# Optimization experiments

Measured on AMD Instinct MI355X. Metric: run time of the kernel, lower is better.

## Reference

```python
import jax, jax.numpy as jnp
import numpy as np

N_ITER = 15
ITER_LR = 0.1


def setup_inputs() -> dict:
    key = jax.random.key(0)
    ks = jax.random.split(key, 4)
    dims = [784, 512, 256, 10]
    x = jax.random.normal(ks[0], (32768, dims[0]), dtype=jnp.float32)
    # weights[i]: (dims[i+1], dims[i]) scaled by sqrt(2/dims[i+1]); biases[i]: (dims[i],) zeros
    W0 = jax.random.normal(ks[1], (dims[1], dims[0]), dtype=jnp.float32) * np.sqrt(2.0 / dims[1]).astype(np.float32)
    W1 = jax.random.normal(ks[2], (dims[2], dims[1]), dtype=jnp.float32) * np.sqrt(2.0 / dims[2]).astype(np.float32)
    W2 = jax.random.normal(ks[3], (dims[3], dims[2]), dtype=jnp.float32) * np.sqrt(2.0 / dims[3]).astype(np.float32)
    b0 = jnp.zeros((dims[0],), dtype=jnp.float32)
    b1 = jnp.zeros((dims[1],), dtype=jnp.float32)
    b2 = jnp.zeros((dims[2],), dtype=jnp.float32)
    return {"x": x, "W0": W0, "W1": W1, "W2": W2, "b0": b0, "b1": b1, "b2": b2}


def reference(x, W0, W1, W2, b0, b1, b2):
    # feedforward pass: mus[i+1] = relu(mus[i] @ W[i].T)
    m1 = jax.nn.relu(x @ W0.T)    # [B, 512]
    m2 = jax.nn.relu(m1 @ W1.T)   # [B, 256]
    m3 = jax.nn.relu(m2 @ W2.T)   # [B, 10]

    # iterative predictive-coding updates: for l in {1, 2}:
    #   pred = relu(mus[l+1] @ W[l] + b[l]); mus[l] = relu(mus[l] - iter_lr * (mus[l] - pred))
    def body(_, carry):
        m1, m2, m3 = carry
        pred1 = jax.nn.relu(m2 @ W1 + b1)                 # uses m2 before its update (loop order)
        m1 = jax.nn.relu(m1 - ITER_LR * (m1 - pred1))
        pred2 = jax.nn.relu(m3 @ W2 + b2)
        m2 = jax.nn.relu(m2 - ITER_LR * (m2 - pred2))
        return (m1, m2, m3)

    m1, m2, m3 = jax.lax.fori_loop(0, N_ITER, body, (m1, m2, m3))
    # mus[-1] is never updated by the loop; returned as-is (faithful to the torch code)
    return m3
```

## Files before the change

kernel.cpp:

```cpp
#include <hip/hip_runtime.h>

typedef __bf16 bhalf;
typedef bhalf bhalf8 __attribute__((ext_vector_type(8)));
typedef float f32x4 __attribute__((ext_vector_type(4)));
typedef unsigned short u16;
typedef u16 u16x8 __attribute__((ext_vector_type(8)));

__device__ __forceinline__ u16 f2bf(float f) {
  union { float f; unsigned u; } v; v.f = f;
  unsigned r = v.u + 0x7FFFu + ((v.u >> 16) & 1u);
  return (u16)(r >> 16);
}

__device__ __forceinline__ int swz(int L) { return L ^ (((L >> 7) & 7) << 4); }

#define GLL16(gp, lp) __builtin_amdgcn_global_load_lds( \
    (const __attribute__((address_space(1))) unsigned int*)(gp), \
    (__attribute__((address_space(3))) unsigned int*)(lp), 16, 0, 0)

#define KP0 800
#define W0E (512 * KP0)
#define W1E (256 * 512)
#define W2E (16 * 256)

__global__ __launch_bounds__(256) void cvt_weights(
    const float* __restrict__ W0, const float* __restrict__ W1,
    const float* __restrict__ W2,
    u16* __restrict__ W0b, u16* __restrict__ W1b, u16* __restrict__ W2b)
{
  int i = blockIdx.x * 256 + threadIdx.x;
  if (i < W0E) {
    int r = i / KP0, k = i - r * KP0;
    W0b[i] = (k < 784) ? f2bf(W0[r * 784 + k]) : (u16)0;
    return;
  }
  i -= W0E;
  if (i < W1E) { W1b[i] = f2bf(W1[i]); return; }
  i -= W1E;
  if (i < W2E) {
    int r = i >> 8, c = i & 255;
    W2b[i] = (r < 10) ? f2bf(W2[r * 256 + c]) : (u16)0;
  }
}

__global__ __launch_bounds__(512) void gemm1_8p(
    const float* __restrict__ x, const u16* __restrict__ Wb, u16* __restrict__ Cp)
{
  __shared__ u16 lds[32768];
  const int t = threadIdx.x, w = t >> 6, lane = t & 63;
  const int bid = blockIdx.x;
  const int rt = (bid & 7) * 16 + (bid >> 4);
  const int ct = (bid >> 3) & 1;
  const size_t rbase = (size_t)rt * 256, cbase = (size_t)ct * 256;
  const int wr = w >> 2, wc = w & 3, fr = lane & 15, fg = lane >> 4;

  int aO[4], bO[4];
#pragma unroll
  for (int m = 0; m < 4; ++m) aO[m] = swz((wr * 128 + m * 16 + fr) * 64 + fg * 16);
#pragma unroll
  for (int n = 0; n < 4; ++n) bO[n] = swz((wc * 64 + n * 16 + fr) * 64 + fg * 16);

  const u16* bSrc[2];
#pragma unroll
  for (int i = 0; i < 2; ++i) {
    int P = (w * 2 + i) * 1024 + lane * 16;
    int U = swz(P);
    bSrc[i] = Wb + (size_t)(cbase + (U >> 6)) * KP0 + ((U & 63) >> 1);
  }

  const float* xRow[2]; int aKe[2];
#pragma unroll
  for (int c2 = 0; c2 < 2; ++c2) {
    int P = c2 * 8192 + t * 16;
    int U = swz(P);
    xRow[c2] = x + (size_t)(rbase + (U >> 6)) * 784;
    aKe[c2] = (U & 63) >> 1;
  }

  f32x4 acc[8][4];
#pragma unroll
  for (int m = 0; m < 8; ++m)
#pragma unroll
    for (int n = 0; n < 4; ++n) acc[m][n] = (f32x4){0.f, 0.f, 0.f, 0.f};

  f32x4 xr[2][2];
  bhalf8 bf[4], afA[4], afB[4];

  auto loadX = [&](int ttn) {
#pragma unroll
    for (int c2 = 0; c2 < 2; ++c2) {
      int gk = ttn * 32 + aKe[c2];
      const float* p = xRow[c2] + ((gk < 784) ? gk : 0);
      xr[c2][0] = *(const f32x4*)p; xr[c2][1] = *(const f32x4*)(p + 4);
    }
  };
  auto cvtW = [&](int aBaseOther) {
#pragma unroll
    for (int c2 = 0; c2 < 2; ++c2) {
      u16x8 v;
#pragma unroll
      for (int j = 0; j < 4; ++j) { v[j] = f2bf(xr[c2][0][j]); v[4 + j] = f2bf(xr[c2][1][j]); }
      *(u16x8*)((char*)lds + aBaseOther + c2 * 8192 + t * 16) = v;
    }
  };
  auto stageB = [&](int ttn, int bBaseT) {
#pragma unroll
    for (int i = 0; i < 2; ++i)
      GLL16(bSrc[i] + ttn * 32, (char*)lds + bBaseT + (w * 2 + i) * 1024);
  };
  auto rdB  = [&](int bB) {
#pragma unroll
    for (int n = 0; n < 4; ++n) bf[n] = *(const bhalf8*)((const char*)lds + bB + bO[n]);
  };
  auto rdA0 = [&](int aB) {
#pragma unroll
    for (int m = 0; m < 4; ++m) afA[m] = *(const bhalf8*)((const char*)lds + aB + aO[m]);
  };
  auto rdA1 = [&](int aB) {
#pragma unroll
    for (int m = 0; m < 4; ++m) afB[m] = *(const bhalf8*)((const char*)lds + aB + aO[m] + 4096);
  };
  auto mfmaLo = [&]() {
    __builtin_amdgcn_s_setprio(1);
#pragma unroll
    for (int m = 0; m < 4; ++m)
#pragma unroll
      for (int n = 0; n < 4; ++n)
        acc[m][n] = __builtin_amdgcn_mfma_f32_16x16x32_bf16(afA[m], bf[n], acc[m][n], 0, 0, 0);
    __builtin_amdgcn_s_setprio(0);
  };
  auto mfmaHi = [&]() {
    __builtin_amdgcn_s_setprio(1);
#pragma unroll
    for (int m = 0; m < 4; ++m)
#pragma unroll
      for (int n = 0; n < 4; ++n)
        acc[4 + m][n] = __builtin_amdgcn_mfma_f32_16x16x32_bf16(afB[m], bf[n], acc[4 + m][n], 0, 0, 0);
    __builtin_amdgcn_s_setprio(0);
  };

  loadX(0);
  stageB(0, 32768);
  cvtW(0);
  loadX(1);
  stageB(1, 49152);
  asm volatile("s_waitcnt vmcnt(6) lgkmcnt(0)" ::: "memory");
  __builtin_amdgcn_s_barrier();

  for (int tt = 0; tt < 23; ++tt) {
    const int c = tt & 1;
    const int aB = c << 14;
    const int bB = 32768 + (c << 14);
    rdB(bB); rdA0(aB); rdA1(aB);
    mfmaLo();
    asm volatile("s_waitcnt lgkmcnt(0)" ::: "memory");
    __builtin_amdgcn_s_barrier();
    cvtW(aB ^ 16384);
    loadX(tt + 2);
    stageB(tt + 2, bB);
    mfmaHi();
    asm volatile("s_waitcnt vmcnt(6) lgkmcnt(0)" ::: "memory");
    __builtin_amdgcn_s_barrier();
  }
  {
    rdB(49152); rdA0(16384); rdA1(16384);
    mfmaLo();
    asm volatile("s_waitcnt lgkmcnt(0)" ::: "memory");
    __builtin_amdgcn_s_barrier();
    cvtW(0);
    mfmaHi();
    asm volatile("s_waitcnt vmcnt(0) lgkmcnt(0)" ::: "memory");
    __builtin_amdgcn_s_barrier();

    rdB(32768); rdA0(0); rdA1(0);
    mfmaLo();
    rdA1(0);
    mfmaHi();
  }

#pragma unroll
  for (int m = 0; m < 8; ++m)
#pragma unroll
    for (int n = 0; n < 4; ++n)
#pragma unroll
      for (int q = 0; q < 4; ++q) {
        size_t row = rbase + wr * 128 + m * 16 + fg * 4 + q;
        size_t col = cbase + wc * 64 + n * 16 + fr;
        float vv = acc[m][n][q];
        vv = vv > 0.f ? vv : 0.f;
        Cp[row * 512 + col] = f2bf(vv);
      }
}

__global__ __launch_bounds__(512, 4) void gemm23(
    const u16* __restrict__ m1, const u16* __restrict__ W1b,
    const u16* __restrict__ W2b, float* __restrict__ out)
{
  __shared__ u16 pool[20480];
  __shared__ u16 W2s[16][264];
  const int t = threadIdx.x, w = t >> 6, lane = t & 63;
  const size_t rbase = (size_t)blockIdx.x * 64;
  const int wr = w >> 2, wc = w & 3, fr = lane & 15, fg = lane >> 4;

  {
    int r = t >> 5, kc = (t & 31) * 8;
    *(int4*)&W2s[r][kc] = *(const int4*)(W2b + r * 256 + kc);
  }

  int aOff[2], bOff[4];
#pragma unroll
  for (int i = 0; i < 2; ++i) aOff[i] = swz((wr * 32 + i * 16 + fr) * 64 + fg * 16);
#pragma unroll
  for (int j = 0; j < 4; ++j) bOff[j] = swz((wc * 64 + j * 16 + fr) * 64 + fg * 16);

  const u16* aSrc = nullptr; int aDst = 0;
  if (w < 4) {
    int Dl = (w * 64 + lane) * 16;
    int Ul = swz(Dl);
    aSrc = m1 + (rbase + (Ul >> 6)) * 512 + ((Ul & 63) >> 1);
    aDst = (w * 64) * 16;
  }
  const u16* bSrc[2]; int bDst[2];
#pragma unroll
  for (int i = 0; i < 2; ++i) {
    int Dl = (w * 128 + i * 64 + lane) * 16;
    int Ul = swz(Dl);
    bSrc[i] = W1b + (Ul >> 6) * 512 + ((Ul & 63) >> 1);
    bDst[i] = 8192 + (w * 128 + i * 64) * 16;
  }

  f32x4 acc[2][4];
#pragma unroll
  for (int i = 0; i < 2; ++i)
#pragma unroll
    for (int j = 0; j < 4; ++j) acc[i][j] = (f32x4){0.f, 0.f, 0.f, 0.f};

  if (w < 4) GLL16(aSrc, (char*)pool + aDst);
#pragma unroll
  for (int i = 0; i < 2; ++i) GLL16(bSrc[i], (char*)pool + bDst[i]);

  for (int tt = 0; tt < 16; ++tt) {
    const int cur = tt & 1;
    const char* Asc = (const char*)pool + cur * 4096;
    const char* Bsc = (const char*)pool + 8192 + cur * 16384;
    asm volatile("s_waitcnt vmcnt(0)" ::: "memory");
    __syncthreads();

    if (tt < 15) {
      const int k0 = (tt + 1) * 32;
      if (w < 4) GLL16(aSrc + k0, (char*)pool + (cur ^ 1) * 4096 + aDst);
#pragma unroll
      for (int i = 0; i < 2; ++i)
        GLL16(bSrc[i] + k0, (char*)pool + (cur ^ 1) * 16384 + bDst[i]);
    }

    bhalf8 af[2], bfv[4];
#pragma unroll
    for (int i = 0; i < 2; ++i) af[i] = *(const bhalf8*)(Asc + aOff[i]);
#pragma unroll
    for (int j = 0; j < 4; ++j) bfv[j] = *(const bhalf8*)(Bsc + bOff[j]);
#pragma unroll
    for (int i = 0; i < 2; ++i)
#pragma unroll
      for (int j = 0; j < 4; ++j)
        acc[i][j] = __builtin_amdgcn_mfma_f32_16x16x32_bf16(af[i], bfv[j], acc[i][j], 0, 0, 0);
  }

  __syncthreads();
#pragma unroll
  for (int i = 0; i < 2; ++i)
#pragma unroll
    for (int j = 0; j < 4; ++j)
#pragma unroll
      for (int q = 0; q < 4; ++q) {
        int row = wr * 32 + i * 16 + fg * 4 + q;
        int col = wc * 64 + j * 16 + fr;
        float vv = acc[i][j][q];
        vv = vv > 0.f ? vv : 0.f;
        pool[row * 264 + col] = f2bf(vv);
      }
  __syncthreads();

  if (w < 4) {
    f32x4 acc3 = (f32x4){0.f, 0.f, 0.f, 0.f};
    const int arow = w * 16 + fr;
#pragma unroll
    for (int ks = 0; ks < 8; ++ks) {
      bhalf8 a = *(const bhalf8*)&pool[arow * 264 + ks * 32 + fg * 8];
      bhalf8 b = *(const bhalf8*)&W2s[fr][ks * 32 + fg * 8];
      acc3 = __builtin_amdgcn_mfma_f32_16x16x32_bf16(a, b, acc3, 0, 0, 0);
    }
    if (fr < 10) {
#pragma unroll
      for (int q = 0; q < 4; ++q) {
        size_t row = rbase + w * 16 + fg * 4 + q;
        float vv = acc3[q];
        out[row * 10 + fr] = vv > 0.f ? vv : 0.f;
      }
    }
  }
}

extern "C" void kernel_launch(void* const* d_in, const int* in_sizes, int n_in,
                              void* d_out, int out_size, void* d_ws, size_t ws_size,
                              hipStream_t stream) {
  const float* x  = (const float*)d_in[0];
  const float* W0 = (const float*)d_in[1];
  const float* W1 = (const float*)d_in[2];
  const float* W2 = (const float*)d_in[3];
  float* out = (float*)d_out;

  char* ws = (char*)d_ws;
  u16* m1  = (u16*)(ws);
  u16* W0b = (u16*)(ws + 33554432);
  u16* W1b = (u16*)(ws + 34373632);
  u16* W2b = (u16*)(ws + 34635776);

  cvt_weights<<<dim3((W0E + W1E + W2E + 255) / 256), dim3(256), 0, stream>>>(
      W0, W1, W2, W0b, W1b, W2b);

  gemm1_8p<<<dim3(256), dim3(512), 0, stream>>>(x, W0b, m1);

  gemm23<<<dim3(512), dim3(512), 0, stream>>>(m1, W1b, W2b, out);
}
```

Baseline: 62.26 us.

## Retile first GEMM to full-width 128x512 tiles so each block reads x once

The first-layer GEMM changes from 256x256 output tiles (two column blocks per row tile) to 128-row tiles that span all 512 output columns. Each block now loads and converts its slice of the fp32 input exactly once, removing the duplicated x traffic and bf16 conversion that came from splitting columns across blocks. Each warp computes 4x8 MFMA fragments, and the B buffers grow, so LDS moves to 80KB of dynamic shared memory, set each launch through hipFuncSetAttribute. The cost is a larger per-block weight stream and heavier LDS use, which can limit occupancy to one block per CU.

```diff
diff --git a/kernel.cpp b/kernel.cpp
--- a/kernel.cpp
+++ b/kernel.cpp
@@ -43,82 +43,68 @@
   }
 }
 
-__global__ __launch_bounds__(512) void gemm1_8p(
+__global__ __launch_bounds__(512) void gemm1_fn(
     const float* __restrict__ x, const u16* __restrict__ Wb, u16* __restrict__ Cp)
 {
-  __shared__ u16 lds[32768];
+  extern __shared__ u16 lds[];
   const int t = threadIdx.x, w = t >> 6, lane = t & 63;
-  const int bid = blockIdx.x;
-  const int rt = (bid & 7) * 16 + (bid >> 4);
-  const int ct = (bid >> 3) & 1;
-  const size_t rbase = (size_t)rt * 256, cbase = (size_t)ct * 256;
+  const size_t rbase = (size_t)blockIdx.x * 128;
   const int wr = w >> 2, wc = w & 3, fr = lane & 15, fg = lane >> 4;
 
-  int aO[4], bO[4];
-#pragma unroll
-  for (int m = 0; m < 4; ++m) aO[m] = swz((wr * 128 + m * 16 + fr) * 64 + fg * 16);
-#pragma unroll
-  for (int n = 0; n < 4; ++n) bO[n] = swz((wc * 64 + n * 16 + fr) * 64 + fg * 16);
-
-  const u16* bSrc[2];
-#pragma unroll
-  for (int i = 0; i < 2; ++i) {
-    int P = (w * 2 + i) * 1024 + lane * 16;
+  int aO[4], bO[8];
+#pragma unroll
+  for (int m = 0; m < 4; ++m) aO[m] = swz((wr * 64 + m * 16 + fr) * 64 + fg * 16);
+#pragma unroll
+  for (int n = 0; n < 8; ++n) bO[n] = swz((wc * 128 + n * 16 + fr) * 64 + fg * 16);
+
+  const u16* bSrc[4];
+#pragma unroll
+  for (int i = 0; i < 4; ++i) {
+    int P = (w * 4 + i) * 1024 + lane * 16;
     int U = swz(P);
-    bSrc[i] = Wb + (size_t)(cbase + (U >> 6)) * KP0 + ((U & 63) >> 1);
-  }
-
-  const float* xRow[2]; int aKe[2];
-#pragma unroll
-  for (int c2 = 0; c2 < 2; ++c2) {
-    int P = c2 * 8192 + t * 16;
+    bSrc[i] = Wb + (size_t)(U >> 6) * KP0 + ((U & 63) >> 1);
+  }
+
+  const float* xRow; int aKe;
+  {
+    int P = t * 16;
     int U = swz(P);
-    xRow[c2] = x + (size_t)(rbase + (U >> 6)) * 784;
-    aKe[c2] = (U & 63) >> 1;
-  }
-
-  f32x4 acc[8][4];
-#pragma unroll
-  for (int m = 0; m < 8; ++m)
-#pragma unroll
-    for (int n = 0; n < 4; ++n) acc[m][n] = (f32x4){0.f, 0.f, 0.f, 0.f};
-
-  f32x4 xr[2][2];
-  bhalf8 bf[4], afA[4], afB[4];
-
-  auto loadX = [&](int ttn) {
-#pragma unroll
-    for (int c2 = 0; c2 < 2; ++c2) {
-      int gk = ttn * 32 + aKe[c2];
-      const float* p = xRow[c2] + ((gk < 784) ? gk : 0);
-      xr[c2][0] = *(const f32x4*)p; xr[c2][1] = *(const f32x4*)(p + 4);
-    }
-  };
-  auto cvtW = [&](int aBaseOther) {
-#pragma unroll
-    for (int c2 = 0; c2 < 2; ++c2) {
-      u16x8 v;
-#pragma unroll
-      for (int j = 0; j < 4; ++j) { v[j] = f2bf(xr[c2][0][j]); v[4 + j] = f2bf(xr[c2][1][j]); }
-      *(u16x8*)((char*)lds + aBaseOther + c2 * 8192 + t * 16) = v;
-    }
-  };
-  auto stageB = [&](int ttn, int bBaseT) {
-#pragma unroll
-    for (int i = 0; i < 2; ++i)
-      GLL16(bSrc[i] + ttn * 32, (char*)lds + bBaseT + (w * 2 + i) * 1024);
-  };
-  auto rdB  = [&](int bB) {
-#pragma unroll
-    for (int n = 0; n < 4; ++n) bf[n] = *(const bhalf8*)((const char*)lds + bB + bO[n]);
-  };
-  auto rdA0 = [&](int aB) {
+    xRow = x + (rbase + (U >> 6)) * (size_t)784;
+    aKe = (U & 63) >> 1;
+  }
+
+  f32x4 acc[4][8];
+#pragma unroll
+  for (int m = 0; m < 4; ++m)
+#pragma unroll
+    for (int n = 0; n < 8; ++n) acc[m][n] = (f32x4){0.f, 0.f, 0.f, 0.f};
+
+  f32x4 xr0, xr1;
+  bhalf8 bf[8], afA[4];
+
+  auto loadX = [&](int s) {
+    int gk = s * 32 + aKe;
+    const float* p = xRow + ((gk < 784) ? gk : 0);
+    xr0 = *(const f32x4*)p; xr1 = *(const f32x4*)(p + 4);
+  };
+  auto cvtW = [&](int aBase) {
+    u16x8 v;
+#pragma unroll
+    for (int j = 0; j < 4; ++j) { v[j] = f2bf(xr0[j]); v[4 + j] = f2bf(xr1[j]); }
+    *(u16x8*)((char*)lds + aBase + t * 16) = v;
+  };
+  auto stageB = [&](int s, int bBase) {
+#pragma unroll
+    for (int i = 0; i < 4; ++i)
+      GLL16(bSrc[i] + s * 32, (char*)lds + bBase + (w * 4 + i) * 1024);
+  };
+  auto rdA = [&](int aB) {
 #pragma unroll
     for (int m = 0; m < 4; ++m) afA[m] = *(const bhalf8*)((const char*)lds + aB + aO[m]);
   };
-  auto rdA1 = [&](int aB) {
-#pragma unroll
-    for (int m = 0; m < 4; ++m) afB[m] = *(const bhalf8*)((const char*)lds + aB + aO[m] + 4096);
+  auto rdB = [&](int bB) {
+#pragma unroll
+    for (int n = 0; n < 8; ++n) bf[n] = *(const bhalf8*)((const char*)lds + bB + bO[n]);
   };
   auto mfmaLo = [&]() {
     __builtin_amdgcn_s_setprio(1);
@@ -134,28 +120,28 @@
 #pragma unroll
     for (int m = 0; m < 4; ++m)
 #pragma unroll
-      for (int n = 0; n < 4; ++n)
-        acc[4 + m][n] = __builtin_amdgcn_mfma_f32_16x16x32_bf16(afB[m], bf[n], acc[4 + m][n], 0, 0, 0);
+      for (int n = 4; n < 8; ++n)
+        acc[m][n] = __builtin_amdgcn_mfma_f32_16x16x32_bf16(afA[m], bf[n], acc[m][n], 0, 0, 0);
     __builtin_amdgcn_s_setprio(0);
   };
 
   loadX(0);
-  stageB(0, 32768);
+  stageB(0, 16384);
   cvtW(0);
   loadX(1);
-  stageB(1, 49152);
+  stageB(1, 16384 + 32768);
   asm volatile("s_waitcnt vmcnt(6) lgkmcnt(0)" ::: "memory");
   __builtin_amdgcn_s_barrier();
 
   for (int tt = 0; tt < 23; ++tt) {
     const int c = tt & 1;
-    const int aB = c << 14;
-    const int bB = 32768 + (c << 14);
-    rdB(bB); rdA0(aB); rdA1(aB);
+    const int aB = c * 8192;
+    const int bB = 16384 + c * 32768;
+    rdA(aB); rdB(bB);
     mfmaLo();
     asm volatile("s_waitcnt lgkmcnt(0)" ::: "memory");
     __builtin_amdgcn_s_barrier();
-    cvtW(aB ^ 16384);
+    cvtW(aB ^ 8192);
     loadX(tt + 2);
     stageB(tt + 2, bB);
     mfmaHi();
@@ -163,7 +149,7 @@
     __builtin_amdgcn_s_barrier();
   }
   {
-    rdB(49152); rdA0(16384); rdA1(16384);
+    rdA(8192); rdB(16384 + 32768);
     mfmaLo();
     asm volatile("s_waitcnt lgkmcnt(0)" ::: "memory");
     __builtin_amdgcn_s_barrier();
@@ -172,20 +158,19 @@
     asm volatile("s_waitcnt vmcnt(0) lgkmcnt(0)" ::: "memory");
     __builtin_amdgcn_s_barrier();
 
-    rdB(32768); rdA0(0); rdA1(0);
+    rdA(0); rdB(16384);
     mfmaLo();
-    rdA1(0);
     mfmaHi();
   }
 
 #pragma unroll
-  for (int m = 0; m < 8; ++m)
-#pragma unroll
-    for (int n = 0; n < 4; ++n)
+  for (int m = 0; m < 4; ++m)
+#pragma unroll
+    for (int n = 0; n < 8; ++n)
 #pragma unroll
       for (int q = 0; q < 4; ++q) {
-        size_t row = rbase + wr * 128 + m * 16 + fg * 4 + q;
-        size_t col = cbase + wc * 64 + n * 16 + fr;
+        size_t row = rbase + wr * 64 + m * 16 + fg * 4 + q;
+        size_t col = (size_t)wc * 128 + n * 16 + fr;
         float vv = acc[m][n][q];
         vv = vv > 0.f ? vv : 0.f;
         Cp[row * 512 + col] = f2bf(vv);
@@ -316,10 +301,13 @@
   u16* W1b = (u16*)(ws + 34373632);
   u16* W2b = (u16*)(ws + 34635776);
 
+  hipFuncSetAttribute((const void*)gemm1_fn,
+                      hipFuncAttributeMaxDynamicSharedMemorySize, 81920);
+
   cvt_weights<<<dim3((W0E + W1E + W2E + 255) / 256), dim3(256), 0, stream>>>(
       W0, W1, W2, W0b, W1b, W2b);
 
-  gemm1_8p<<<dim3(256), dim3(512), 0, stream>>>(x, W0b, m1);
+  gemm1_fn<<<dim3(256), dim3(512), 81920, stream>>>(x, W0b, m1);
 
   gemm23<<<dim3(512), dim3(512), 0, stream>>>(m1, W1b, W2b, out);
 }
```

After: 65.64 us. +5.4%, slower.
